# Performance work log

Hardware: AMD Instinct MI355X
Metric: run time of the kernel (lower is better)

## Reference

```python
import jax, jax.numpy as jnp
import numpy as np

TEMPERATURE = 0.1
WINDOW = 7  # torch loop: k in range(1, min(8, seq_len - i)) -> offsets 1..7


def _normalize(x, axis=-1, eps=1e-12):
    # F.normalize: x / max(||x||, eps)
    n = jnp.linalg.norm(x, axis=axis, keepdims=True)
    return x / jnp.maximum(n, eps)


def setup_inputs() -> dict:
    key = jax.random.key(0)
    k1, k2 = jax.random.split(key, 2)
    states = jax.random.normal(k1, (4, 16, 1024, 256), dtype=jnp.float32)
    patterns = jax.random.normal(k2, (64, 256), dtype=jnp.float32)
    transfer_weights = jnp.zeros((16, 64, 64), dtype=jnp.float32)
    return {"states": states, "patterns": patterns, "transfer_weights": transfer_weights}


def _forward(states, patterns, transfer_weights):
    b, h, s, d = states.shape
    # --- detect_patterns: similarity to normalized pattern library + softmax ---
    sims = jnp.einsum('bhsd,pd->bhsp', states, _normalize(patterns))
    pattern_scores = jax.nn.softmax(sims / TEMPERATURE, axis=-1)  # [b,h,s,p]

    # --- compute_routing_scores: grad of states.sum() wrt states is ones ->
    #     grad_norm = ||ones||_2 over dim = sqrt(d) (constant), softmax over seq ---
    grad_norm = jnp.full((b, h, s), jnp.sqrt(jnp.float32(d)), dtype=states.dtype)
    routing_scores = jax.nn.softmax(grad_norm / TEMPERATURE, axis=-1)  # uniform [b,h,s]

    # --- optimize_routing: windowed min-plus shortest-path DP ---
    # torch keeps distances [b,h,s,s] but every slice along dim 2 is identical
    # (init and updates only index the last axis), so carry a [b,h,s] vector
    # and broadcast at the end. Pad by WINDOW so near-end updates land in pad.
    inf = jnp.float32(np.inf)
    dist0 = jnp.full((b, h, s + WINDOW), inf, dtype=states.dtype).at[..., 0].set(0.0)
    cost_pad = jnp.pad(-routing_scores, ((0, 0), (0, 0), (0, WINDOW)))

    def step(dist, i):
        cur = jax.lax.dynamic_slice_in_dim(dist, i, 1, axis=-1)          # [b,h,1]
        win = jax.lax.dynamic_slice_in_dim(dist, i + 1, WINDOW, axis=-1)  # [b,h,W]
        c = jax.lax.dynamic_slice_in_dim(cost_pad, i + 1, WINDOW, axis=-1)
        new = jnp.minimum(win, cur + c)
        dist = jax.lax.dynamic_update_slice_in_dim(dist, new, i + 1, axis=-1)
        return dist, None

    dist, _ = jax.lax.scan(step, dist0, jnp.arange(s - 1))
    d_final = dist[..., :s]                                  # [b,h,s]
    optimal_routes = jnp.broadcast_to(d_final[:, :, None, :], (b, h, s, s))

    return routing_scores, optimal_routes, transfer_weights, pattern_scores


def reference(states, patterns, transfer_weights):
    return _forward(states, patterns, transfer_weights)
```

## Files before the change

kernel.cpp:

```cpp
#include <hip/hip_runtime.h>
#include <math.h>

constexpr int B = 4, H = 16, S = 1024, D = 256, P = 64;
constexpr long long N_ROWS = (long long)B * H * S;
constexpr long long OFF_RT = 0;
constexpr long long SZ_RT  = N_ROWS;
constexpr long long OFF_OR = OFF_RT + SZ_RT;
constexpr long long SZ_OR  = N_ROWS * (long long)S;
constexpr long long OFF_TW = OFF_OR + SZ_OR;
constexpr long long SZ_TW  = 16LL * 64 * 64;
constexpr long long OFF_PS = OFF_TW + SZ_TW;

typedef _Float16 half8  __attribute__((ext_vector_type(8)));
typedef _Float16 half4v __attribute__((ext_vector_type(4)));
typedef float    floatx4 __attribute__((ext_vector_type(4)));

__global__ __launch_bounds__(64) void k_normalize(const float* __restrict__ pat,
                                                  _Float16* __restrict__ pnh,
                                                  _Float16* __restrict__ pnl) {
    int p    = blockIdx.x;
    int lane = threadIdx.x;
    const float4* src = (const float4*)(pat + (long long)p * D);
    float4 v = src[lane];
    float ss = v.x * v.x + v.y * v.y + v.z * v.z + v.w * v.w;
    #pragma unroll
    for (int m = 1; m < 64; m <<= 1) ss += __shfl_xor(ss, m, 64);
    float scale = 10.0f / fmaxf(sqrtf(ss), 1e-12f);
    float a[4] = { v.x * scale, v.y * scale, v.z * scale, v.w * scale };
    half4v hh, ll;
    #pragma unroll
    for (int j = 0; j < 4; ++j) {
        _Float16 h = (_Float16)a[j];
        hh[j] = h;
        ll[j] = (_Float16)(a[j] - (float)h);
    }
    *(half4v*)(pnh + (long long)p * D + lane * 4) = hh;
    *(half4v*)(pnl + (long long)p * D + lane * 4) = ll;
}

__global__ __launch_bounds__(256) void k_small(const float* __restrict__ tw,
                                               float* __restrict__ out) {
    int i = blockIdx.x * 256 + threadIdx.x;
    if (i < (int)SZ_RT) {
        out[OFF_RT + i] = 0.0009765625f;
    } else {
        int j = i - (int)SZ_RT;
        out[OFF_TW + j] = tw[j];
    }
}

__global__ __launch_bounds__(256) void k_routes(float4* __restrict__ out) {
    long long i = (long long)blockIdx.x * 256 + threadIdx.x;
    int j0 = (int)((i << 2) & (S - 1));
    float b0 = (float)j0 * (-0.0009765625f);
    float4 v;
    v.x = b0;
    v.y = b0 - 0.0009765625f;
    v.z = b0 - 0.001953125f;
    v.w = b0 - 0.0029296875f;
    out[i] = v;
}

__global__ __launch_bounds__(256) void k_gemm_mfma(
        const float* __restrict__ states,
        const _Float16* __restrict__ pnh,
        const _Float16* __restrict__ pnl,
        float* __restrict__ out_ps) {
    int wave = threadIdx.x >> 6;
    int lane = threadIdx.x & 63;
    int q    = lane >> 4;
    int m    = lane & 15;
    long long row0 = (long long)blockIdx.x * 64 + wave * 16;
    const float* __restrict__ arow = states + (row0 + m) * D + q * 8;

    floatx4 acc[4] = {floatx4{0,0,0,0}, floatx4{0,0,0,0},
                      floatx4{0,0,0,0}, floatx4{0,0,0,0}};

    #pragma unroll 2
    for (int kk = 0; kk < 8; ++kk) {
        float4 a0 = *(const float4*)(arow + kk * 32);
        float4 a1 = *(const float4*)(arow + kk * 32 + 4);
        float av[8] = { a0.x, a0.y, a0.z, a0.w, a1.x, a1.y, a1.z, a1.w };
        half8 ah, al;
        #pragma unroll
        for (int j = 0; j < 8; ++j) {
            _Float16 h = (_Float16)av[j];
            ah[j] = h;
            al[j] = (_Float16)(av[j] - (float)h);
        }
        #pragma unroll
        for (int t = 0; t < 4; ++t) {
            long long boff = (long long)(t * 16 + m) * D + kk * 32 + q * 8;
            half8 bh = *(const half8*)(pnh + boff);
            half8 bl = *(const half8*)(pnl + boff);
            acc[t] = __builtin_amdgcn_mfma_f32_16x16x32_f16(ah, bh, acc[t], 0, 0, 0);
            acc[t] = __builtin_amdgcn_mfma_f32_16x16x32_f16(al, bh, acc[t], 0, 0, 0);
            acc[t] = __builtin_amdgcn_mfma_f32_16x16x32_f16(ah, bl, acc[t], 0, 0, 0);
        }
    }

    float e[4][4];
    #pragma unroll
    for (int r = 0; r < 4; ++r) {
        float mx = fmaxf(fmaxf(acc[0][r], acc[1][r]), fmaxf(acc[2][r], acc[3][r]));
        #pragma unroll
        for (int msk = 1; msk < 16; msk <<= 1) mx = fmaxf(mx, __shfl_xor(mx, msk, 64));
        float s = 0.0f;
        #pragma unroll
        for (int t = 0; t < 4; ++t) { e[t][r] = __expf(acc[t][r] - mx); s += e[t][r]; }
        #pragma unroll
        for (int msk = 1; msk < 16; msk <<= 1) s += __shfl_xor(s, msk, 64);
        float inv = 1.0f / s;
        long long row = row0 + q * 4 + r;
        #pragma unroll
        for (int t = 0; t < 4; ++t) {
            out_ps[row * P + t * 16 + m] = e[t][r] * inv;
        }
    }
}

extern "C" void kernel_launch(void* const* d_in, const int* in_sizes, int n_in,
                              void* d_out, int out_size, void* d_ws, size_t ws_size,
                              hipStream_t stream) {
    const float* states   = (const float*)d_in[0];
    const float* patterns = (const float*)d_in[1];
    const float* transfer = (const float*)d_in[2];
    float* out = (float*)d_out;
    _Float16* pnh = (_Float16*)d_ws;
    _Float16* pnl = pnh + P * D;

    k_normalize<<<dim3(P), dim3(64), 0, stream>>>(patterns, pnh, pnl);

    k_small<<<dim3(512), dim3(256), 0, stream>>>(transfer, out);

    k_routes<<<dim3(65536), dim3(256), 0, stream>>>((float4*)(out + OFF_OR));

    k_gemm_mfma<<<dim3(1024), dim3(256), 0, stream>>>(states, pnh, pnl, out + OFF_PS);
}
```

Baseline: 345.5 us.

## Fuse route fill, small outputs and pattern GEMM into one kernel

Merges the routing-score fill, the transfer-weight copy, the 256 MB optimal_routes broadcast fill and the MFMA pattern-score GEMM into a single kernel with 1024 blocks. Each block writes 64 rows of routes with nontemporal stores alongside its GEMM work. States are read with nontemporal loads. This removes two launches and lets the store-bound fill overlap the GEMM, but it puts a large serial store loop in each block ahead of its MFMA work.

```diff
diff --git a/kernel.cpp b/kernel.cpp
--- a/kernel.cpp
+++ b/kernel.cpp
@@ -11,8 +11,8 @@
 constexpr long long SZ_TW  = 16LL * 64 * 64;
 constexpr long long OFF_PS = OFF_TW + SZ_TW;
 
-typedef _Float16 half8  __attribute__((ext_vector_type(8)));
-typedef _Float16 half4v __attribute__((ext_vector_type(4)));
+typedef _Float16 half8   __attribute__((ext_vector_type(8)));
+typedef _Float16 half4v  __attribute__((ext_vector_type(4)));
 typedef float    floatx4 __attribute__((ext_vector_type(4)));
 
 __global__ __launch_bounds__(64) void k_normalize(const float* __restrict__ pat,
@@ -20,8 +20,8 @@
                                                   _Float16* __restrict__ pnl) {
     int p    = blockIdx.x;
     int lane = threadIdx.x;
-    const float4* src = (const float4*)(pat + (long long)p * D);
-    float4 v = src[lane];
+    const floatx4* src = (const floatx4*)(pat + (long long)p * D);
+    floatx4 v = src[lane];
     float ss = v.x * v.x + v.y * v.y + v.z * v.z + v.w * v.w;
     #pragma unroll
     for (int m = 1; m < 64; m <<= 1) ss += __shfl_xor(ss, m, 64);
@@ -38,39 +38,39 @@
     *(half4v*)(pnl + (long long)p * D + lane * 4) = ll;
 }
 
-__global__ __launch_bounds__(256) void k_small(const float* __restrict__ tw,
-                                               float* __restrict__ out) {
-    int i = blockIdx.x * 256 + threadIdx.x;
-    if (i < (int)SZ_RT) {
-        out[OFF_RT + i] = 0.0009765625f;
-    } else {
-        int j = i - (int)SZ_RT;
-        out[OFF_TW + j] = tw[j];
-    }
-}
-
-__global__ __launch_bounds__(256) void k_routes(float4* __restrict__ out) {
-    long long i = (long long)blockIdx.x * 256 + threadIdx.x;
-    int j0 = (int)((i << 2) & (S - 1));
-    float b0 = (float)j0 * (-0.0009765625f);
-    float4 v;
-    v.x = b0;
-    v.y = b0 - 0.0009765625f;
-    v.z = b0 - 0.001953125f;
-    v.w = b0 - 0.0029296875f;
-    out[i] = v;
-}
-
-__global__ __launch_bounds__(256) void k_gemm_mfma(
+__global__ __launch_bounds__(256) void k_fused(
         const float* __restrict__ states,
         const _Float16* __restrict__ pnh,
         const _Float16* __restrict__ pnl,
-        float* __restrict__ out_ps) {
-    int wave = threadIdx.x >> 6;
-    int lane = threadIdx.x & 63;
+        const float* __restrict__ tw,
+        float* __restrict__ out) {
+    const int  t   = threadIdx.x;
+    const long long blk = blockIdx.x;
+
+    if (t < 64) {
+        out[OFF_RT + blk * 64 + t] = 0.0009765625f;
+        out[OFF_TW + blk * 64 + t] = tw[blk * 64 + t];
+    }
+
+    {
+        float b0 = (float)(t * 4) * (-0.0009765625f);
+        floatx4 v;
+        v.x = b0;
+        v.y = b0 - 0.0009765625f;
+        v.z = b0 - 0.001953125f;
+        v.w = b0 - 0.0029296875f;
+        floatx4* dst = (floatx4*)(out + OFF_OR + blk * 64 * (long long)S) + t;
+        #pragma unroll 8
+        for (int i = 0; i < 64; ++i) {
+            __builtin_nontemporal_store(v, dst + i * 256);
+        }
+    }
+
+    int wave = t >> 6;
+    int lane = t & 63;
     int q    = lane >> 4;
     int m    = lane & 15;
-    long long row0 = (long long)blockIdx.x * 64 + wave * 16;
+    long long row0 = blk * 64 + wave * 16;
     const float* __restrict__ arow = states + (row0 + m) * D + q * 8;
 
     floatx4 acc[4] = {floatx4{0,0,0,0}, floatx4{0,0,0,0},
@@ -78,8 +78,8 @@
 
     #pragma unroll 2
     for (int kk = 0; kk < 8; ++kk) {
-        float4 a0 = *(const float4*)(arow + kk * 32);
-        float4 a1 = *(const float4*)(arow + kk * 32 + 4);
+        floatx4 a0 = __builtin_nontemporal_load((const floatx4*)(arow + kk * 32));
+        floatx4 a1 = __builtin_nontemporal_load((const floatx4*)(arow + kk * 32 + 4));
         float av[8] = { a0.x, a0.y, a0.z, a0.w, a1.x, a1.y, a1.z, a1.w };
         half8 ah, al;
         #pragma unroll
@@ -89,13 +89,13 @@
             al[j] = (_Float16)(av[j] - (float)h);
         }
         #pragma unroll
-        for (int t = 0; t < 4; ++t) {
-            long long boff = (long long)(t * 16 + m) * D + kk * 32 + q * 8;
+        for (int tt = 0; tt < 4; ++tt) {
+            long long boff = (long long)(tt * 16 + m) * D + kk * 32 + q * 8;
             half8 bh = *(const half8*)(pnh + boff);
             half8 bl = *(const half8*)(pnl + boff);
-            acc[t] = __builtin_amdgcn_mfma_f32_16x16x32_f16(ah, bh, acc[t], 0, 0, 0);
-            acc[t] = __builtin_amdgcn_mfma_f32_16x16x32_f16(al, bh, acc[t], 0, 0, 0);
-            acc[t] = __builtin_amdgcn_mfma_f32_16x16x32_f16(ah, bl, acc[t], 0, 0, 0);
+            acc[tt] = __builtin_amdgcn_mfma_f32_16x16x32_f16(ah, bh, acc[tt], 0, 0, 0);
+            acc[tt] = __builtin_amdgcn_mfma_f32_16x16x32_f16(al, bh, acc[tt], 0, 0, 0);
+            acc[tt] = __builtin_amdgcn_mfma_f32_16x16x32_f16(ah, bl, acc[tt], 0, 0, 0);
         }
     }
 
@@ -107,14 +107,14 @@
         for (int msk = 1; msk < 16; msk <<= 1) mx = fmaxf(mx, __shfl_xor(mx, msk, 64));
         float s = 0.0f;
         #pragma unroll
-        for (int t = 0; t < 4; ++t) { e[t][r] = __expf(acc[t][r] - mx); s += e[t][r]; }
+        for (int tt = 0; tt < 4; ++tt) { e[tt][r] = __expf(acc[tt][r] - mx); s += e[tt][r]; }
         #pragma unroll
         for (int msk = 1; msk < 16; msk <<= 1) s += __shfl_xor(s, msk, 64);
         float inv = 1.0f / s;
         long long row = row0 + q * 4 + r;
         #pragma unroll
-        for (int t = 0; t < 4; ++t) {
-            out_ps[row * P + t * 16 + m] = e[t][r] * inv;
+        for (int tt = 0; tt < 4; ++tt) {
+            out[OFF_PS + row * P + tt * 16 + m] = e[tt][r] * inv;
         }
     }
 }
@@ -131,9 +131,5 @@
 
     k_normalize<<<dim3(P), dim3(64), 0, stream>>>(patterns, pnh, pnl);
 
-    k_small<<<dim3(512), dim3(256), 0, stream>>>(transfer, out);
-
-    k_routes<<<dim3(65536), dim3(256), 0, stream>>>((float4*)(out + OFF_OR));
-
-    k_gemm_mfma<<<dim3(1024), dim3(256), 0, stream>>>(states, pnh, pnl, out + OFF_PS);
+    k_fused<<<dim3(1024), dim3(256), 0, stream>>>(states, pnh, pnl, transfer, out);
 }
```

After: 354.8 us. 1.03x slower.
